# Kernel tuning notes

Hardware: AMD Instinct MI355X
Metric: run time of the kernel (lower is better)

## Reference

```python
import jax, jax.numpy as jnp
import numpy as np

N = 100000      # nodes
E = 1000000     # edges
IN = 64         # in_dim
TD = 64         # time_dim
OUT = 64        # out_dim
H = 4           # num_heads
HD = OUT // H   # head_dim = 16


def setup_inputs() -> dict:
    key = jax.random.key(0)
    ks = jax.random.split(key, 12)
    g = lambda k, shp, s: (jax.random.normal(k, shp, jnp.float32) * s)
    return {
        "x": g(ks[0], (N, IN), 1.0),
        "time_features": g(ks[1], (N, TD), 1.0),
        "edge_index": jax.random.randint(ks[2], (2, E), 0, N, dtype=jnp.int32),
        # nn.Linear weights stored as [in, out] (already transposed)
        "q_w": g(ks[3], (IN + TD, OUT), 0.05), "q_b": g(ks[4], (OUT,), 0.05),
        "k_w": g(ks[5], (IN + TD, OUT), 0.05), "k_b": g(ks[6], (OUT,), 0.05),
        "v_w": g(ks[7], (IN, OUT), 0.05),      "v_b": g(ks[8], (OUT,), 0.05),
        "o_w": g(ks[9], (OUT, OUT), 0.05),     "o_b": g(ks[10], (OUT,), 0.05),
    }


def reference(x, time_features, edge_index, q_w, q_b, k_w, k_b, v_w, v_b, o_w, o_b):
    xt = jnp.concatenate([x, time_features], axis=-1)            # [N, IN+TD]
    Q = (xt @ q_w + q_b).reshape(N, H, HD)
    K = (xt @ k_w + k_b).reshape(N, H, HD)
    V = (x @ v_w + v_b).reshape(N, H, HD)
    src, dst = edge_index[0], edge_index[1]
    # edge-gather QK dot-product: [E, H]
    scores = jnp.sum(Q[dst] * K[src], axis=-1) / np.float32(np.sqrt(HD))
    # per-destination (segment) softmax over edges, numerically stable two-pass
    seg_max = jax.ops.segment_max(scores, dst, num_segments=N)   # [N, H]
    e = jnp.exp(scores - seg_max[dst])                           # [E, H]
    seg_sum = jax.ops.segment_sum(e, dst, num_segments=N)        # [N, H]
    attn = e / seg_sum[dst]                                      # [E, H]
    # weighted scatter-add of values
    messages = attn[..., None] * V[src]                          # [E, H, HD]
    out = jax.ops.segment_sum(messages, dst, num_segments=N)     # [N, H, HD]
    out = out.reshape(N, OUT)
    return out @ o_w + o_b
```

## Files before the change

### kernel.cpp

```cpp
#include <hip/hip_runtime.h>
#include <hip/hip_fp16.h>
#include <math.h>

#define N_NODES 100000
#define N_EDGES 1000000
#define QKV_BLOCKS ((N_NODES + 63) / 64)
#define FILL_BLOCKS ((N_EDGES + 255) / 256)
#define PREP_BLOCKS 96
#define AGG_BLOCKS (N_NODES / 32)

typedef __attribute__((ext_vector_type(8))) _Float16 f16x8;
typedef __attribute__((ext_vector_type(4))) float    f32x4;

__global__ __launch_bounds__(256) void prep_kernel(
    const float* __restrict__ qw, const float* __restrict__ kw,
    const float* __restrict__ vw, const float* __restrict__ ow,
    _Float16* __restrict__ WqT, _Float16* __restrict__ WkT,
    _Float16* __restrict__ WvT, _Float16* __restrict__ WoT)
{
    const int idx = blockIdx.x * 256 + threadIdx.x;
    if (idx < 8192) {
        const int c = idx >> 7, k = idx & 127;
        WqT[idx] = (_Float16)qw[k * 64 + c];
    } else if (idx < 16384) {
        const int i = idx - 8192, c = i >> 7, k = i & 127;
        WkT[i] = (_Float16)kw[k * 64 + c];
    } else if (idx < 20480) {
        const int i = idx - 16384, c = i >> 6, k = i & 63;
        WvT[i] = (_Float16)vw[k * 64 + c];
    } else {
        const int i = idx - 20480, c = i >> 6, k = i & 63;
        WoT[i] = (_Float16)ow[k * 64 + c];
    }
}

__global__ __launch_bounds__(256) void fill_qkv_kernel(
    const int* __restrict__ src, const int* __restrict__ dst,
    int* __restrict__ head, int2* __restrict__ next2,
    const float* __restrict__ x, const float* __restrict__ tf,
    const _Float16* __restrict__ WqT, const _Float16* __restrict__ WkT,
    const _Float16* __restrict__ WvT,
    const float* __restrict__ qb, const float* __restrict__ kb,
    const float* __restrict__ vb,
    _Float16* __restrict__ Qh, _Float16* __restrict__ Kh,
    _Float16* __restrict__ Vh)
{
    __shared__ _Float16 xt[64][128];
    const int t = threadIdx.x;

    if (blockIdx.x >= QKV_BLOCKS) {
        const int e = (blockIdx.x - QKV_BLOCKS) * 256 + t;
        if (e < N_EDGES) {
            const int d  = dst[e];
            const int sv = src[e];
            const int old = atomicExch(&head[d], e);
            next2[e] = make_int2(old, sv);
        }
        return;
    }

    const int base = blockIdx.x * 64;

    {
        const int j = t & 15;
        #pragma unroll
        for (int i = 0; i < 4; ++i) {
            const int r = (t >> 4) + 16 * i;
            int node = base + r;
            if (node >= N_NODES) node = N_NODES - 1;
            const float* p = (j < 8) ? (x  + (size_t)node * 64 + 8 * j)
                                     : (tf + (size_t)node * 64 + 8 * (j - 8));
            const float4 lo = ((const float4*)p)[0];
            const float4 hi = ((const float4*)p)[1];
            f16x8 h = { (_Float16)lo.x, (_Float16)lo.y, (_Float16)lo.z,
                        (_Float16)lo.w, (_Float16)hi.x, (_Float16)hi.y,
                        (_Float16)hi.z, (_Float16)hi.w };
            const int js = j ^ (r & 15);
            *(f16x8*)&xt[r][js * 8] = h;
        }
    }

    const int wave = t >> 6;
    const int lane = t & 63;
    const int lrow = lane & 15;
    const int lgrp = lane >> 4;
    const int cw   = wave * 16;

    f16x8 bq[4], bk[4], bv[2];
    const float biasq = qb[cw + lrow];
    const float biask = kb[cw + lrow];
    const float biasv = vb[cw + lrow];
    {
        const size_t rq = (size_t)(cw + lrow) * 128 + lgrp * 8;
        #pragma unroll
        for (int kt = 0; kt < 4; ++kt) {
            bq[kt] = *(const f16x8*)&WqT[rq + kt * 32];
            bk[kt] = *(const f16x8*)&WkT[rq + kt * 32];
        }
        const size_t rv = (size_t)(cw + lrow) * 64 + lgrp * 8;
        #pragma unroll
        for (int kt = 0; kt < 2; ++kt)
            bv[kt] = *(const f16x8*)&WvT[rv + kt * 32];
    }
    __syncthreads();

    #pragma unroll
    for (int rt = 0; rt < 4; ++rt) {
        f16x8 a[4];
        const int r = rt * 16 + lrow;
        #pragma unroll
        for (int kt = 0; kt < 4; ++kt) {
            const int js = (kt * 4 + lgrp) ^ lrow;
            a[kt] = *(const f16x8*)&xt[r][js * 8];
        }
        f32x4 accq = {0.f, 0.f, 0.f, 0.f};
        f32x4 acck = {0.f, 0.f, 0.f, 0.f};
        f32x4 accv = {0.f, 0.f, 0.f, 0.f};
        #pragma unroll
        for (int kt = 0; kt < 4; ++kt) {
            accq = __builtin_amdgcn_mfma_f32_16x16x32_f16(a[kt], bq[kt], accq, 0, 0, 0);
            acck = __builtin_amdgcn_mfma_f32_16x16x32_f16(a[kt], bk[kt], acck, 0, 0, 0);
        }
        #pragma unroll
        for (int kt = 0; kt < 2; ++kt)
            accv = __builtin_amdgcn_mfma_f32_16x16x32_f16(a[kt], bv[kt], accv, 0, 0, 0);
        #pragma unroll
        for (int rr = 0; rr < 4; ++rr) {
            const int node = base + rt * 16 + lgrp * 4 + rr;
            if (node < N_NODES) {
                const size_t o = (size_t)node * 64 + cw + lrow;
                Qh[o] = (_Float16)(accq[rr] + biasq);
                Kh[o] = (_Float16)(acck[rr] + biask);
                Vh[o] = (_Float16)(accv[rr] + biasv);
            }
        }
    }
}

__global__ __launch_bounds__(256) void agg_kernel(
    const int* __restrict__ head, const int2* __restrict__ next2,
    const __half* __restrict__ Qh, const __half* __restrict__ Kh,
    const __half* __restrict__ Vh,
    const _Float16* __restrict__ WoT, const float* __restrict__ ob,
    float* __restrict__ out)
{
    __shared__ _Float16 aggh[32][64];
    const int wave = threadIdx.x >> 6;
    const int lane = threadIdx.x & 63;
    const int g    = lane >> 3;
    const int s    = lane & 7;
    const int lrow = lane & 15;
    const int lgrp = lane >> 4;
    const int cw   = wave * 16;
    const int nb   = blockIdx.x * 32;
    const int node = nb + wave * 8 + g;

    f16x8 bo0, bo1;
    {
        const size_t ro = (size_t)(cw + lrow) * 64 + lgrp * 8;
        bo0 = *(const f16x8*)&WoT[ro];
        bo1 = *(const f16x8*)&WoT[ro + 32];
    }
    const float biaso = ob[cw + lrow];

    const uint4* __restrict__ Q4 = (const uint4*)Qh;
    const uint4* __restrict__ K4 = (const uint4*)Kh;
    const uint4* __restrict__ V4 = (const uint4*)Vh;

    float qf[8];
    {
        const uint4 qu = Q4[(size_t)node * 8 + s];
        const __half2* qh = (const __half2*)&qu;
        #pragma unroll
        for (int j = 0; j < 4; ++j) {
            const float2 a = __half22float2(qh[j]);
            qf[2 * j] = a.x; qf[2 * j + 1] = a.y;
        }
    }

    float acc[8] = {0.f, 0.f, 0.f, 0.f, 0.f, 0.f, 0.f, 0.f};
    float ssum = 0.f;

    int e = head[node];
    bool act = (e >= 0);
    while (__any(act)) {
        const int es = act ? e : 0;
        const int2 sn = next2[es];
        const int sv = sn.y;
        const uint4 ku = K4[(size_t)sv * 8 + s];
        const uint4 vu = V4[(size_t)sv * 8 + s];

        float kf[8], vf[8];
        {
            const __half2* kh = (const __half2*)&ku;
            const __half2* vh = (const __half2*)&vu;
            #pragma unroll
            for (int j = 0; j < 4; ++j) {
                const float2 a = __half22float2(kh[j]);
                const float2 b = __half22float2(vh[j]);
                kf[2 * j] = a.x; kf[2 * j + 1] = a.y;
                vf[2 * j] = b.x; vf[2 * j + 1] = b.y;
            }
        }
        float dq = qf[0] * kf[0] + qf[1] * kf[1] + qf[2] * kf[2] + qf[3] * kf[3]
                 + qf[4] * kf[4] + qf[5] * kf[5] + qf[6] * kf[6] + qf[7] * kf[7];
        dq += __shfl_xor(dq, 1);
        const float p = act ? __expf(dq * 0.25f) : 0.f;
        ssum += p;
        #pragma unroll
        for (int j = 0; j < 8; ++j) acc[j] = fmaf(p, vf[j], acc[j]);

        e = act ? sn.x : -1;
        act = (e >= 0);
    }

    {
        const float inv = (ssum > 0.f) ? (1.0f / ssum) : 0.0f;
        const int r = wave * 8 + g;
        f16x8 h = { (_Float16)(acc[0] * inv), (_Float16)(acc[1] * inv),
                    (_Float16)(acc[2] * inv), (_Float16)(acc[3] * inv),
                    (_Float16)(acc[4] * inv), (_Float16)(acc[5] * inv),
                    (_Float16)(acc[6] * inv), (_Float16)(acc[7] * inv) };
        *(f16x8*)&aggh[r][(s ^ g) * 8] = h;
    }
    __syncthreads();

    #pragma unroll
    for (int rt = 0; rt < 2; ++rt) {
        const int r = rt * 16 + lrow;
        f16x8 a0 = *(const f16x8*)&aggh[r][((lgrp)     ^ (lrow & 7)) * 8];
        f16x8 a1 = *(const f16x8*)&aggh[r][((4 + lgrp) ^ (lrow & 7)) * 8];
        f32x4 acco = {0.f, 0.f, 0.f, 0.f};
        acco = __builtin_amdgcn_mfma_f32_16x16x32_f16(a0, bo0, acco, 0, 0, 0);
        acco = __builtin_amdgcn_mfma_f32_16x16x32_f16(a1, bo1, acco, 0, 0, 0);
        #pragma unroll
        for (int rr = 0; rr < 4; ++rr) {
            const int n = nb + rt * 16 + lgrp * 4 + rr;
            out[(size_t)n * 64 + cw + lrow] = acco[rr] + biaso;
        }
    }
}

extern "C" void kernel_launch(void* const* d_in, const int* in_sizes, int n_in,
                              void* d_out, int out_size, void* d_ws, size_t ws_size,
                              hipStream_t stream) {
    const float* x  = (const float*)d_in[0];
    const float* tf = (const float*)d_in[1];
    const int*   ei = (const int*)  d_in[2];
    const float* qw = (const float*)d_in[3];
    const float* qb = (const float*)d_in[4];
    const float* kw = (const float*)d_in[5];
    const float* kb = (const float*)d_in[6];
    const float* vw = (const float*)d_in[7];
    const float* vb = (const float*)d_in[8];
    const float* ow = (const float*)d_in[9];
    const float* ob = (const float*)d_in[10];
    float* out = (float*)d_out;

    char* ws = (char*)d_ws;
    const size_t hf = (size_t)N_NODES * 64 * sizeof(_Float16);

    _Float16* Qh      = (_Float16*)(ws);
    _Float16* Kh      = (_Float16*)(ws + hf);
    _Float16* Vh      = (_Float16*)(ws + 2 * hf);
    _Float16* WqT     = (_Float16*)(ws + 3 * hf);
    _Float16* WkT     = WqT + 8192;
    _Float16* WvT     = WkT + 8192;
    _Float16* WoT     = WvT + 4096;
    int*      head    = (int*)(WoT + 4096);
    int2*     next2   = (int2*)(head + N_NODES);

    const int* src = ei;
    const int* dst = ei + N_EDGES;

    const dim3 blk(256);

    hipMemsetAsync(head, 0xFF, N_NODES * sizeof(int), stream);

    prep_kernel<<<dim3(PREP_BLOCKS), blk, 0, stream>>>(
        qw, kw, vw, ow, WqT, WkT, WvT, WoT);

    fill_qkv_kernel<<<dim3(QKV_BLOCKS + FILL_BLOCKS), blk, 0, stream>>>(
        src, dst, head, next2,
        x, tf, WqT, WkT, WvT, qb, kb, vb, Qh, Kh, Vh);

    agg_kernel<<<dim3(AGG_BLOCKS), blk, 0, stream>>>(
        head, next2, (const __half*)Qh, (const __half*)Kh, (const __half*)Vh,
        WoT, ob, out);
}
```

Measured before the change: 140.9 us.

## Dynamic per-wave node work pool and interleaved K/V layout in aggregation

The aggregation kernel now handles 64 nodes per block. Each wave takes 16 nodes from a shared-memory ticket counter, so an 8-lane group that finishes a short edge list immediately claims another node. This reduces the divergence where a whole wave waits on its longest linked list. K and V are also stored interleaved per node, so each edge gather reads from one contiguous 256-byte row. In exchange the loop carries more control flow and LDS atomics, and there are fewer blocks in total.

Result: faster. 131.8 us (-6.4%).

```diff
diff --git a/kernel.cpp b/kernel.cpp
--- a/kernel.cpp
+++ b/kernel.cpp
@@ -7,7 +7,7 @@
 #define QKV_BLOCKS ((N_NODES + 63) / 64)
 #define FILL_BLOCKS ((N_EDGES + 255) / 256)
 #define PREP_BLOCKS 96
-#define AGG_BLOCKS (N_NODES / 32)
+#define AGG_BLOCKS ((N_NODES + 63) / 64)
 
 typedef __attribute__((ext_vector_type(8))) _Float16 f16x8;
 typedef __attribute__((ext_vector_type(4))) float    f32x4;
@@ -42,8 +42,7 @@
     const _Float16* __restrict__ WvT,
     const float* __restrict__ qb, const float* __restrict__ kb,
     const float* __restrict__ vb,
-    _Float16* __restrict__ Qh, _Float16* __restrict__ Kh,
-    _Float16* __restrict__ Vh)
+    _Float16* __restrict__ Qh, _Float16* __restrict__ KV)
 {
     __shared__ _Float16 xt[64][128];
     const int t = threadIdx.x;
@@ -128,10 +127,9 @@
         for (int rr = 0; rr < 4; ++rr) {
             const int node = base + rt * 16 + lgrp * 4 + rr;
             if (node < N_NODES) {
-                const size_t o = (size_t)node * 64 + cw + lrow;
-                Qh[o] = (_Float16)(accq[rr] + biasq);
-                Kh[o] = (_Float16)(acck[rr] + biask);
-                Vh[o] = (_Float16)(accv[rr] + biasv);
+                Qh[(size_t)node * 64 + cw + lrow]        = (_Float16)(accq[rr] + biasq);
+                KV[(size_t)node * 128 + cw + lrow]       = (_Float16)(acck[rr] + biask);
+                KV[(size_t)node * 128 + 64 + cw + lrow]  = (_Float16)(accv[rr] + biasv);
             }
         }
     }
@@ -139,21 +137,24 @@
 
 __global__ __launch_bounds__(256) void agg_kernel(
     const int* __restrict__ head, const int2* __restrict__ next2,
-    const __half* __restrict__ Qh, const __half* __restrict__ Kh,
-    const __half* __restrict__ Vh,
+    const __half* __restrict__ Qh, const __half* __restrict__ KVh,
     const _Float16* __restrict__ WoT, const float* __restrict__ ob,
     float* __restrict__ out)
 {
-    __shared__ _Float16 aggh[32][64];
-    const int wave = threadIdx.x >> 6;
-    const int lane = threadIdx.x & 63;
+    __shared__ _Float16 aggh[64][64];
+    __shared__ int pool[4];
+    const int t    = threadIdx.x;
+    const int wave = t >> 6;
+    const int lane = t & 63;
     const int g    = lane >> 3;
     const int s    = lane & 7;
     const int lrow = lane & 15;
     const int lgrp = lane >> 4;
     const int cw   = wave * 16;
-    const int nb   = blockIdx.x * 32;
-    const int node = nb + wave * 8 + g;
+    const int nb   = blockIdx.x * 64;
+    const int wbase = wave * 16;
+
+    if (lane == 0) pool[wave] = 8;
 
     f16x8 bo0, bo1;
     {
@@ -162,14 +163,21 @@
         bo1 = *(const f16x8*)&WoT[ro + 32];
     }
     const float biaso = ob[cw + lrow];
-
-    const uint4* __restrict__ Q4 = (const uint4*)Qh;
-    const uint4* __restrict__ K4 = (const uint4*)Kh;
-    const uint4* __restrict__ V4 = (const uint4*)Vh;
-
+    __syncthreads();
+
+    const uint4* __restrict__ Q4  = (const uint4*)Qh;
+    const uint4* __restrict__ KV4 = (const uint4*)KVh;
+
+    int   idx  = g;
+    int   cur  = nb + wbase + idx;
+    int   e    = (cur < N_NODES) ? head[cur] : -1;
+    bool  done = false;
+    float acc[8] = {0.f, 0.f, 0.f, 0.f, 0.f, 0.f, 0.f, 0.f};
+    float ssum = 0.f;
     float qf[8];
     {
-        const uint4 qu = Q4[(size_t)node * 8 + s];
+        const int qn = (cur < N_NODES) ? cur : 0;
+        const uint4 qu = Q4[(size_t)qn * 8 + s];
         const __half2* qh = (const __half2*)&qu;
         #pragma unroll
         for (int j = 0; j < 4; ++j) {
@@ -178,17 +186,46 @@
         }
     }
 
-    float acc[8] = {0.f, 0.f, 0.f, 0.f, 0.f, 0.f, 0.f, 0.f};
-    float ssum = 0.f;
-
-    int e = head[node];
-    bool act = (e >= 0);
-    while (__any(act)) {
-        const int es = act ? e : 0;
-        const int2 sn = next2[es];
-        const int sv = sn.y;
-        const uint4 ku = K4[(size_t)sv * 8 + s];
-        const uint4 vu = V4[(size_t)sv * 8 + s];
+    for (;;) {
+        while (e < 0 && !done) {
+            const float inv = (ssum > 0.f) ? (1.0f / ssum) : 0.0f;
+            const int r = wbase + idx;
+            f16x8 h = { (_Float16)(acc[0] * inv), (_Float16)(acc[1] * inv),
+                        (_Float16)(acc[2] * inv), (_Float16)(acc[3] * inv),
+                        (_Float16)(acc[4] * inv), (_Float16)(acc[5] * inv),
+                        (_Float16)(acc[6] * inv), (_Float16)(acc[7] * inv) };
+            *(f16x8*)&aggh[r][(s ^ (r & 7)) * 8] = h;
+
+            int tkt = 0;
+            if (s == 0) tkt = atomicAdd(&pool[wave], 1);
+            tkt = __shfl(tkt, g * 8);
+            if (tkt < 16) {
+                idx = tkt;
+                cur = nb + wbase + idx;
+                e   = (cur < N_NODES) ? head[cur] : -1;
+                const int qn = (cur < N_NODES) ? cur : 0;
+                const uint4 qu = Q4[(size_t)qn * 8 + s];
+                const __half2* qh = (const __half2*)&qu;
+                #pragma unroll
+                for (int j = 0; j < 4; ++j) {
+                    const float2 a = __half22float2(qh[j]);
+                    qf[2 * j] = a.x; qf[2 * j + 1] = a.y;
+                }
+                #pragma unroll
+                for (int j = 0; j < 8; ++j) acc[j] = 0.f;
+                ssum = 0.f;
+            } else {
+                done = true;
+            }
+        }
+        if (__all(done)) break;
+
+        const bool act = (e >= 0);
+        const int  es  = act ? e : 0;
+        const int2 sn  = next2[es];
+        const int  sv  = sn.y;
+        const uint4 ku = KV4[(size_t)sv * 16 + s];
+        const uint4 vu = KV4[(size_t)sv * 16 + 8 + s];
 
         float kf[8], vf[8];
         {
@@ -209,24 +246,12 @@
         ssum += p;
         #pragma unroll
         for (int j = 0; j < 8; ++j) acc[j] = fmaf(p, vf[j], acc[j]);
-
-        e = act ? sn.x : -1;
-        act = (e >= 0);
-    }
-
-    {
-        const float inv = (ssum > 0.f) ? (1.0f / ssum) : 0.0f;
-        const int r = wave * 8 + g;
-        f16x8 h = { (_Float16)(acc[0] * inv), (_Float16)(acc[1] * inv),
-                    (_Float16)(acc[2] * inv), (_Float16)(acc[3] * inv),
-                    (_Float16)(acc[4] * inv), (_Float16)(acc[5] * inv),
-                    (_Float16)(acc[6] * inv), (_Float16)(acc[7] * inv) };
-        *(f16x8*)&aggh[r][(s ^ g) * 8] = h;
+        e = act ? sn.x : e;
     }
     __syncthreads();
 
     #pragma unroll
-    for (int rt = 0; rt < 2; ++rt) {
+    for (int rt = 0; rt < 4; ++rt) {
         const int r = rt * 16 + lrow;
         f16x8 a0 = *(const f16x8*)&aggh[r][((lgrp)     ^ (lrow & 7)) * 8];
         f16x8 a1 = *(const f16x8*)&aggh[r][((4 + lgrp) ^ (lrow & 7)) * 8];
@@ -236,7 +261,8 @@
         #pragma unroll
         for (int rr = 0; rr < 4; ++rr) {
             const int n = nb + rt * 16 + lgrp * 4 + rr;
-            out[(size_t)n * 64 + cw + lrow] = acco[rr] + biaso;
+            if (n < N_NODES)
+                out[(size_t)n * 64 + cw + lrow] = acco[rr] + biaso;
         }
     }
 }
@@ -261,8 +287,7 @@
     const size_t hf = (size_t)N_NODES * 64 * sizeof(_Float16);
 
     _Float16* Qh      = (_Float16*)(ws);
-    _Float16* Kh      = (_Float16*)(ws + hf);
-    _Float16* Vh      = (_Float16*)(ws + 2 * hf);
+    _Float16* KV      = (_Float16*)(ws + hf);
     _Float16* WqT     = (_Float16*)(ws + 3 * hf);
     _Float16* WkT     = WqT + 8192;
     _Float16* WvT     = WkT + 8192;
@@ -282,9 +307,8 @@
 
     fill_qkv_kernel<<<dim3(QKV_BLOCKS + FILL_BLOCKS), blk, 0, stream>>>(
         src, dst, head, next2,
-        x, tf, WqT, WkT, WvT, qb, kb, vb, Qh, Kh, Vh);
+        x, tf, WqT, WkT, WvT, qb, kb, vb, Qh, KV);
 
     agg_kernel<<<dim3(AGG_BLOCKS), blk, 0, stream>>>(
-        head, next2, (const __half*)Qh, (const __half*)Kh, (const __half*)Vh,
-        WoT, ob, out);
+        head, next2, (const __half*)Qh, (const __half*)KV, WoT, ob, out);
 }
```
